# Optimization experiments

Hardware: AMD Instinct MI355X
Metric: run time of the kernel (lower is better)

## Reference

```python
import jax, jax.numpy as jnp
import numpy as np
from jax import lax


def quick_gelu(x):
    return x * jax.nn.sigmoid(1.702 * x)


def setup_inputs() -> dict:
    key = jax.random.key(0)
    ks = jax.random.split(key, 12)
    B, H, W, C, D, M = 32, 56, 56, 192, 64, 8
    g = lambda k, shape, s: (jax.random.normal(k, shape, jnp.float32) * s)
    return {
        "x": jax.random.normal(ks[0], (B, H, W, C), jnp.float32),
        "W1": g(ks[1], (64, C), 0.05),
        "b1": jnp.zeros((64,), jnp.float32),
        "W2": g(ks[2], (64, 64), 0.05),
        "b2": jnp.zeros((64,), jnp.float32),
        "mask_token": g(ks[3], (M, 64), 0.05),
        "Wh": g(ks[4], (D * D * 9, 64), 0.02),
        "bh": g(ks[5], (D * D * 9,), 0.02),
        "Wd": g(ks[6], (D, C), 0.05),
        "bd": jnp.zeros((D,), jnp.float32),
        "Wu": g(ks[7], (C, D), 0.02),
        "bu": jnp.zeros((C,), jnp.float32),
    }


def reference(x, W1, b1, W2, b2, mask_token, Wh, bh, Wd, bd, Wu, bu):
    B, H, W_, C = x.shape
    D = Wd.shape[0]
    M = mask_token.shape[0]
    # meta_net: Linear -> ReLU -> Linear, [B,H,W,64]
    pf = jax.nn.relu(jnp.einsum("bhwc,kc->bhwk", x, W1) + b1)
    pf = jnp.einsum("bhwk,jk->bhwj", pf, W2) + b2
    # mask routing: [M,B,H,W], softmax over spatial positions
    mask = jnp.einsum("bhwk,mk->mbhw", pf, mask_token)
    mask = jax.nn.softmax(mask.reshape(M, B, -1), axis=-1).reshape(M, B, H, W_)
    # sum_m mask[m][...,None]*pf, then sum over H,W -> [B,64]
    mwf = (mask.sum(0)[..., None] * pf).sum(axis=(1, 2))
    # hypernet: per-sample conv weights [B,D,D,3,3]
    conv_w = (jnp.einsum("bk,ok->bo", mwf, Wh) + bh).reshape(B, D, D, 3, 3)
    # adapter_down + QuickGELU, [B,D,H,W]
    xd = jnp.einsum("bhwc,dc->bhwd", x, Wd) + bd
    xp = quick_gelu(xd.transpose(0, 3, 1, 2))

    def conv1(xi, wi):  # xi [D,H,W], wi [D,D,3,3]
        return lax.conv_general_dilated(xi[None], wi, (1, 1), [(1, 1), (1, 1)])[0]

    xc = jax.vmap(conv1)(xp, conv_w)  # [B,D,H,W]
    xd2 = quick_gelu(xc.transpose(0, 2, 3, 1))  # [B,H,W,D]
    # dropout(p=0.1) is identity in eval mode
    xu = jnp.einsum("bhwd,cd->bhwc", xd2, Wu) + bu
    return xu + x
```

## Files before the change

kernel.cpp:

```cpp
#include <hip/hip_runtime.h>

typedef unsigned short ushort_t;
typedef short bf16x8 __attribute__((ext_vector_type(8)));
typedef float f32x4 __attribute__((ext_vector_type(4)));

#define MFMA(a, b, c) __builtin_amdgcn_mfma_f32_16x16x32_bf16(a, b, c, 0, 0, 0)

#define B_    32
#define HW_   3136
#define NPOS  100352

__device__ __forceinline__ float bf2f(unsigned short h) {
    return __uint_as_float(((unsigned int)h) << 16);
}
__device__ __forceinline__ unsigned short f2bf(float f) {
    unsigned int u = __float_as_uint(f);
    u += 0x7FFFu + ((u >> 16) & 1u);
    return (unsigned short)(u >> 16);
}
__device__ __forceinline__ float qgelu(float v) {
    return v / (1.0f + __expf(-1.702f * v));
}
__device__ __forceinline__ void unpack8(uint4 v, float* f) {
    f[0] = bf2f((unsigned short)(v.x & 0xffff)); f[1] = bf2f((unsigned short)(v.x >> 16));
    f[2] = bf2f((unsigned short)(v.y & 0xffff)); f[3] = bf2f((unsigned short)(v.y >> 16));
    f[4] = bf2f((unsigned short)(v.z & 0xffff)); f[5] = bf2f((unsigned short)(v.z >> 16));
    f[6] = bf2f((unsigned short)(v.w & 0xffff)); f[7] = bf2f((unsigned short)(v.w >> 16));
}

__global__ __launch_bounds__(256) void k0_prep(
    const float* __restrict__ W1, const float* __restrict__ W2,
    const float* __restrict__ mtok, const float* __restrict__ Wd,
    const float* __restrict__ Wu,
    ushort_t* __restrict__ w1f, ushort_t* __restrict__ wdf,
    ushort_t* __restrict__ w2f, ushort_t* __restrict__ mtf,
    ushort_t* __restrict__ wuf)
{
    const int gid = blockIdx.x * 256 + threadIdx.x;
    const int stride = gridDim.x * 256;
    for (int i = gid; i < 12288; i += stride) {
        int j = i & 7, lane = (i >> 3) & 63, nt = (i >> 9) & 3, kc = i >> 11;
        int n = nt * 16 + (lane & 15), k = kc * 32 + (lane >> 4) * 8 + j;
        w1f[i] = f2bf(W1[n * 192 + k]);
        wdf[i] = f2bf(Wd[n * 192 + k]);
    }
    for (int i = gid; i < 4096; i += stride) {
        int j = i & 7, lane = (i >> 3) & 63, nt = (i >> 9) & 3, kc = i >> 11;
        int n = nt * 16 + (lane & 15), k = kc * 32 + (lane >> 4) * 8 + j;
        w2f[i] = f2bf(W2[n * 64 + k]);
    }
    for (int i = gid; i < 1024; i += stride) {
        int j = i & 7, lane = (i >> 3) & 63, kc = i >> 9;
        int n = lane & 15, k = kc * 32 + (lane >> 4) * 8 + j;
        mtf[i] = (n < 8) ? f2bf(mtok[n * 64 + k]) : (ushort_t)0;
    }
    for (int i = gid; i < 12288; i += stride) {
        int j = i & 7, lane = (i >> 3) & 63, g = i >> 9;
        int nt = g % 12, kc = g / 12;
        int n = nt * 16 + (lane & 15), k = kc * 32 + (lane >> 4) * 8 + j;
        wuf[i] = f2bf(Wu[n * 64 + k]);
    }
}

__global__ __launch_bounds__(256, 2) void k1_meta_adapter(
    const float* __restrict__ x, const float* __restrict__ b1,
    const float* __restrict__ b2, const float* __restrict__ bd,
    const ushort_t* __restrict__ w1f, const ushort_t* __restrict__ wdf,
    const ushort_t* __restrict__ w2f, const ushort_t* __restrict__ mtf,
    ushort_t* __restrict__ pf2g, ushort_t* __restrict__ xpg,
    float* __restrict__ Lg)
{
    __shared__ ushort_t wsh[29696];
    __shared__ ushort_t buf[4][16 * 72];

    const int tid = threadIdx.x;
    const int lane = tid & 63, wv = tid >> 6;
    const int col = lane & 15, q = lane >> 4;
    const int posBase = blockIdx.x * 64;
    const float* xrow = x + (size_t)(posBase + wv * 16 + col) * 192;

    float4 xv[6][2];
    #pragma unroll
    for (int kc = 0; kc < 6; kc++) {
        const float4* gp = (const float4*)(xrow + kc * 32 + q * 8);
        xv[kc][0] = gp[0]; xv[kc][1] = gp[1];
    }

    {
        uint4* d = (uint4*)wsh;
        const uint4* s1 = (const uint4*)w1f;
        for (int u = tid; u < 1536; u += 256) d[u] = s1[u];
        uint4* d2 = (uint4*)(wsh + 12288);
        const uint4* s2 = (const uint4*)wdf;
        for (int u = tid; u < 1536; u += 256) d2[u] = s2[u];
        uint4* d3 = (uint4*)(wsh + 24576);
        const uint4* s3 = (const uint4*)w2f;
        for (int u = tid; u < 512; u += 256) d3[u] = s3[u];
        uint4* d4 = (uint4*)(wsh + 28672);
        const uint4* s4 = (const uint4*)mtf;
        if (tid < 128) d4[tid] = s4[tid];
    }

    bf16x8 A[6];
    #pragma unroll
    for (int kc = 0; kc < 6; kc++) {
        float4 v0 = xv[kc][0], v1 = xv[kc][1];
        A[kc][0] = (short)f2bf(v0.x); A[kc][1] = (short)f2bf(v0.y);
        A[kc][2] = (short)f2bf(v0.z); A[kc][3] = (short)f2bf(v0.w);
        A[kc][4] = (short)f2bf(v1.x); A[kc][5] = (short)f2bf(v1.y);
        A[kc][6] = (short)f2bf(v1.z); A[kc][7] = (short)f2bf(v1.w);
    }
    __syncthreads();

    f32x4 acc1[4], acc3[4];
    #pragma unroll
    for (int nt = 0; nt < 4; nt++) { acc1[nt] = (f32x4)0.0f; acc3[nt] = (f32x4)0.0f; }

    #pragma unroll
    for (int kc = 0; kc < 6; kc++) {
        #pragma unroll
        for (int nt = 0; nt < 4; nt++) {
            bf16x8 B1 = *(const bf16x8*)&wsh[((kc * 4 + nt) * 64 + lane) * 8];
            acc1[nt] = MFMA(A[kc], B1, acc1[nt]);
            bf16x8 Bd = *(const bf16x8*)&wsh[12288 + ((kc * 4 + nt) * 64 + lane) * 8];
            acc3[nt] = MFMA(A[kc], Bd, acc3[nt]);
        }
    }

    ushort_t* bA = &buf[wv][0];

    #pragma unroll
    for (int nt = 0; nt < 4; nt++) {
        float bias = b1[nt * 16 + col];
        #pragma unroll
        for (int r = 0; r < 4; r++) {
            float v = acc1[nt][r] + bias;
            v = v > 0.0f ? v : 0.0f;
            bA[(q * 4 + r) * 72 + nt * 16 + col] = f2bf(v);
        }
    }

    f32x4 acc2[4];
    #pragma unroll
    for (int nt = 0; nt < 4; nt++) acc2[nt] = (f32x4)0.0f;
    #pragma unroll
    for (int kc = 0; kc < 2; kc++) {
        bf16x8 A2 = *(const bf16x8*)&bA[col * 72 + kc * 32 + q * 8];
        #pragma unroll
        for (int nt = 0; nt < 4; nt++) {
            bf16x8 B2 = *(const bf16x8*)&wsh[24576 + ((kc * 4 + nt) * 64 + lane) * 8];
            acc2[nt] = MFMA(A2, B2, acc2[nt]);
        }
    }

    #pragma unroll
    for (int nt = 0; nt < 4; nt++) {
        float bias = bd[nt * 16 + col];
        #pragma unroll
        for (int r = 0; r < 4; r++) {
            float v = qgelu(acc3[nt][r] + bias);
            bA[(q * 4 + r) * 72 + nt * 16 + col] = f2bf(v);
        }
    }

    #pragma unroll
    for (int t = 0; t < 2; t++) {
        int idx = lane + t * 64;
        int pos = idx >> 3, c8 = idx & 7;
        uint4 vx = *(const uint4*)&bA[pos * 72 + c8 * 8];
        *(uint4*)(xpg + ((size_t)(posBase + wv * 16 + pos)) * 64 + c8 * 8) = vx;
    }

    #pragma unroll
    for (int nt = 0; nt < 4; nt++) {
        float bias = b2[nt * 16 + col];
        #pragma unroll
        for (int r = 0; r < 4; r++)
            bA[(q * 4 + r) * 72 + nt * 16 + col] = f2bf(acc2[nt][r] + bias);
    }

    f32x4 Lacc = (f32x4)0.0f;
    #pragma unroll
    for (int kc = 0; kc < 2; kc++) {
        bf16x8 A3 = *(const bf16x8*)&bA[col * 72 + kc * 32 + q * 8];
        bf16x8 Bm = *(const bf16x8*)&wsh[28672 + (kc * 64 + lane) * 8];
        Lacc = MFMA(A3, Bm, Lacc);
    }
    if (col < 8) {
        #pragma unroll
        for (int r = 0; r < 4; r++)
            Lg[((size_t)(posBase + wv * 16 + q * 4 + r)) * 8 + col] = Lacc[r];
    }

    #pragma unroll
    for (int t = 0; t < 2; t++) {
        int idx = lane + t * 64;
        int pos = idx >> 3, c8 = idx & 7;
        uint4 vp = *(const uint4*)&bA[pos * 72 + c8 * 8];
        *(uint4*)(pf2g + ((size_t)(posBase + wv * 16 + pos)) * 64 + c8 * 8) = vp;
    }
}

__global__ __launch_bounds__(256) void k2a_partial(
    const float* __restrict__ Lg, float* __restrict__ Pmax, float* __restrict__ Psum)
{
    __shared__ float wred[4][8];
    __shared__ float Msh[8];

    const int tid = threadIdx.x;
    const int b = blockIdx.x >> 3, sl = blockIdx.x & 7;
    const int lane = tid & 63, wv = tid >> 6;
    const float* Lb = Lg + ((size_t)b * HW_ + (size_t)sl * 392) * 8;

    float l0[8], l1[8];
    {
        const float4* p = (const float4*)(Lb + (size_t)tid * 8);
        float4 a = p[0], c = p[1];
        l0[0] = a.x; l0[1] = a.y; l0[2] = a.z; l0[3] = a.w;
        l0[4] = c.x; l0[5] = c.y; l0[6] = c.z; l0[7] = c.w;
    }
    if (tid < 136) {
        const float4* p = (const float4*)(Lb + (size_t)(tid + 256) * 8);
        float4 a = p[0], c = p[1];
        l1[0] = a.x; l1[1] = a.y; l1[2] = a.z; l1[3] = a.w;
        l1[4] = c.x; l1[5] = c.y; l1[6] = c.z; l1[7] = c.w;
    } else {
        #pragma unroll
        for (int m = 0; m < 8; m++) l1[m] = -1e30f;
    }

    float lm[8];
    #pragma unroll
    for (int m = 0; m < 8; m++) {
        float v = fmaxf(l0[m], l1[m]);
        for (int off = 32; off > 0; off >>= 1) v = fmaxf(v, __shfl_down(v, off));
        lm[m] = v;
    }
    if (lane == 0) {
        #pragma unroll
        for (int m = 0; m < 8; m++) wred[wv][m] = lm[m];
    }
    __syncthreads();
    if (tid < 8)
        Msh[tid] = fmaxf(fmaxf(wred[0][tid], wred[1][tid]), fmaxf(wred[2][tid], wred[3][tid]));
    __syncthreads();

    float s[8];
    #pragma unroll
    for (int m = 0; m < 8; m++)
        s[m] = __expf(l0[m] - Msh[m]) + __expf(l1[m] - Msh[m]);
    #pragma unroll
    for (int m = 0; m < 8; m++) {
        float v = s[m];
        for (int off = 32; off > 0; off >>= 1) v += __shfl_down(v, off);
        s[m] = v;
    }
    __syncthreads();
    if (lane == 0) {
        #pragma unroll
        for (int m = 0; m < 8; m++) wred[wv][m] = s[m];
    }
    __syncthreads();
    if (tid < 8) {
        Psum[((size_t)b * 8 + sl) * 8 + tid] =
            wred[0][tid] + wred[1][tid] + wred[2][tid] + wred[3][tid];
        Pmax[((size_t)b * 8 + sl) * 8 + tid] = Msh[tid];
    }
}

__global__ __launch_bounds__(256) void k2b_combine(
    const float* __restrict__ Pmax, const float* __restrict__ Psum,
    float* __restrict__ smxg, float* __restrict__ sinvg, float* __restrict__ mwfg)
{
    const int tid = threadIdx.x;
    const int b = tid >> 3, m = tid & 7;
    float M = -1e30f;
    #pragma unroll
    for (int sl = 0; sl < 8; sl++)
        M = fmaxf(M, Pmax[((size_t)b * 8 + sl) * 8 + m]);
    float S = 0.0f;
    #pragma unroll
    for (int sl = 0; sl < 8; sl++)
        S += Psum[((size_t)b * 8 + sl) * 8 + m] * __expf(Pmax[((size_t)b * 8 + sl) * 8 + m] - M);
    smxg[tid] = M;
    sinvg[tid] = 1.0f / S;
    for (int i = tid; i < 2048; i += 256) mwfg[i] = 0.0f;
}

__global__ __launch_bounds__(256) void k2c_mwf(
    const float* __restrict__ Lg, const ushort_t* __restrict__ pf2g,
    const float* __restrict__ smxg, const float* __restrict__ sinvg,
    float* __restrict__ mwfg)
{
    __shared__ float ms[392];
    __shared__ float sred[32 * 64];

    const int tid = threadIdx.x;
    const int b = blockIdx.x >> 3, sl = blockIdx.x & 7;
    const size_t base = (size_t)b * HW_ + (size_t)sl * 392;

    float smx[8], sinv[8];
    #pragma unroll
    for (int m = 0; m < 8; m++) {
        smx[m] = smxg[b * 8 + m];
        sinv[m] = sinvg[b * 8 + m];
    }

    for (int lp = tid; lp < 392; lp += 256) {
        const float4* p = (const float4*)(Lg + (base + lp) * 8);
        float4 a = p[0], c = p[1];
        ms[lp] = __expf(a.x - smx[0]) * sinv[0] + __expf(a.y - smx[1]) * sinv[1]
               + __expf(a.z - smx[2]) * sinv[2] + __expf(a.w - smx[3]) * sinv[3]
               + __expf(c.x - smx[4]) * sinv[4] + __expf(c.y - smx[5]) * sinv[5]
               + __expf(c.z - smx[6]) * sinv[6] + __expf(c.w - smx[7]) * sinv[7];
    }
    __syncthreads();

    const int part = tid >> 3, kg = tid & 7;
    float a8[8];
    #pragma unroll
    for (int j = 0; j < 8; j++) a8[j] = 0.0f;
    for (int lp = part; lp < 392; lp += 32) {
        float w = ms[lp];
        uint4 v = *(const uint4*)(pf2g + (base + lp) * 64 + kg * 8);
        float f[8]; unpack8(v, f);
        #pragma unroll
        for (int j = 0; j < 8; j++) a8[j] += w * f[j];
    }
    #pragma unroll
    for (int j = 0; j < 8; j++) sred[part * 64 + kg * 8 + j] = a8[j];
    __syncthreads();
    if (tid < 64) {
        float s = 0.0f;
        #pragma unroll
        for (int pt = 0; pt < 32; pt++) s += sred[pt * 64 + tid];
        atomicAdd(&mwfg[b * 64 + tid], s);
    }
}

__global__ __launch_bounds__(256) void k3_hypernet(
    const float* __restrict__ mwfg, const float* __restrict__ Whg,
    const float* __restrict__ bhg, ushort_t* __restrict__ cwb)
{
    __shared__ float mwfs[32 * 64];
    const int tid = threadIdx.x;
    for (int i = tid; i < 2048; i += 256) mwfs[i] = mwfg[i];
    __syncthreads();

    const int op = blockIdx.x * 64 + (tid >> 2);
    const int bq = tid & 3;
    const int j = op & 7, lane = (op >> 3) & 63, nt = (op >> 9) & 3;
    const int kc = (op >> 11) & 1, tap = op >> 12;
    const int oc = nt * 16 + (lane & 15);
    const int ic = kc * 32 + (lane >> 4) * 8 + j;
    const int o = oc * 576 + ic * 9 + tap;

    float wreg[64];
    const float4* src = (const float4*)(Whg + (size_t)o * 64);
    #pragma unroll
    for (int t = 0; t < 16; t++) {
        float4 v = src[t];
        wreg[t * 4 + 0] = v.x; wreg[t * 4 + 1] = v.y;
        wreg[t * 4 + 2] = v.z; wreg[t * 4 + 3] = v.w;
    }
    const float bias = bhg[o];
    #pragma unroll
    for (int i = 0; i < 8; i += 2) {
        int b0 = bq * 8 + i, b1 = b0 + 1;
        float a0 = bias, a1 = bias;
        #pragma unroll
        for (int k = 0; k < 64; k++) {
            a0 += mwfs[b0 * 64 + k] * wreg[k];
            a1 += mwfs[b1 * 64 + k] * wreg[k];
        }
        cwb[(size_t)b0 * 36864 + op] = f2bf(a0);
        cwb[(size_t)b1 * 36864 + op] = f2bf(a1);
    }
}

__global__ __launch_bounds__(256, 4) void k4_conv(
    const ushort_t* __restrict__ xpg, const ushort_t* __restrict__ cwb,
    ushort_t* __restrict__ xd2g)
{
    __shared__ ushort_t xs[2 * 232 * 40];

    const int tid = threadIdx.x;
    const int bid = blockIdx.x;
    const int swz = (bid & 7) * 112 + (bid >> 3);
    const int b = swz / 28, yt = swz % 28, y0 = yt * 2;

    for (int u = tid; u < 1856; u += 256) {
        int r = u / 464, rem = u % 464, c = rem >> 3, c8 = rem & 7;
        int gy = y0 - 1 + r, gx = c - 1;
        uint4 v = make_uint4(0, 0, 0, 0);
        if (gy >= 0 && gy < 56 && gx >= 0 && gx < 56)
            v = *(const uint4*)(xpg + ((size_t)b * HW_ + gy * 56 + gx) * 64 + c8 * 8);
        int kc = c8 >> 2, q = c8 & 3;
        *(uint4*)&xs[kc * 9280 + (r * 58 + c) * 40 + q * 8] = v;
    }
    __syncthreads();

    const int lane = tid & 63, wv = tid >> 6;
    const int col = lane & 15, q = lane >> 4;

    int abase[7];
    #pragma unroll
    for (int t = 0; t < 7; t++) {
        int p = t * 16 + col;
        int row = p / 56, cc = p - row * 56;
        abase[t] = ((row * 58 + cc) * 40 + q * 8) * 2;
    }

    f32x4 acc[7];
    #pragma unroll
    for (int t = 0; t < 7; t++) acc[t] = (f32x4)0.0f;

    const ushort_t* wbase = cwb + (size_t)b * 36864;
    #pragma unroll
    for (int tap = 0; tap < 9; tap++) {
        const int dy = tap / 3, dx = tap % 3;
        const int toff = (dy * 58 + dx) * 80;
        bf16x8 Bf0 = *(const bf16x8*)(wbase + tap * 4096 + ((0 * 4 + wv) * 64 + lane) * 8);
        bf16x8 Bf1 = *(const bf16x8*)(wbase + tap * 4096 + ((1 * 4 + wv) * 64 + lane) * 8);
        #pragma unroll
        for (int t = 0; t < 7; t++) {
            bf16x8 A0 = *(const bf16x8*)((const char*)xs + abase[t] + toff);
            bf16x8 A1 = *(const bf16x8*)((const char*)xs + 18560 + abase[t] + toff);
            acc[t] = MFMA(A0, Bf0, acc[t]);
            acc[t] = MFMA(A1, Bf1, acc[t]);
        }
    }
    __syncthreads();

    #pragma unroll
    for (int t = 0; t < 7; t++)
        #pragma unroll
        for (int r = 0; r < 4; r++)
            xs[(t * 16 + q * 4 + r) * 72 + wv * 16 + col] = f2bf(qgelu(acc[t][r]));
    __syncthreads();

    for (int u = tid; u < 896; u += 256) {
        int pos = u >> 3, c8 = u & 7;
        uint4 v = *(const uint4*)&xs[pos * 72 + c8 * 8];
        size_t gpos = (size_t)b * HW_ + (size_t)y0 * 56 + pos;
        *(uint4*)(xd2g + gpos * 64 + c8 * 8) = v;
    }
}

__global__ __launch_bounds__(256, 4) void k5_up_res(
    const ushort_t* __restrict__ xd2g, const ushort_t* __restrict__ wuf,
    const float* __restrict__ bu, const float* __restrict__ xg,
    float* __restrict__ outg)
{
    __shared__ ushort_t xds[64 * 72];
    __shared__ ushort_t wsh[12288];

    const int tid = threadIdx.x;
    const size_t posBase = (size_t)blockIdx.x * 64;

    {
        uint4* d = (uint4*)wsh;
        const uint4* s = (const uint4*)wuf;
        for (int u = tid; u < 1536; u += 256) d[u] = s[u];
    }
    #pragma unroll
    for (int t = 0; t < 2; t++) {
        int u = tid + t * 256;
        int pos = u >> 3, c8 = u & 7;
        uint4 v = *(const uint4*)(xd2g + (posBase + pos) * 64 + c8 * 8);
        *(uint4*)&xds[pos * 72 + c8 * 8] = v;
    }
    __syncthreads();

    const int lane = tid & 63, wv = tid >> 6;
    const int col = lane & 15, q = lane >> 4;

    bf16x8 A[2];
    #pragma unroll
    for (int kc = 0; kc < 2; kc++)
        A[kc] = *(const bf16x8*)&xds[(wv * 16 + col) * 72 + kc * 32 + q * 8];

    f32x4 acc[12];
    #pragma unroll
    for (int nt = 0; nt < 12; nt++) acc[nt] = (f32x4)0.0f;
    #pragma unroll
    for (int kc = 0; kc < 2; kc++)
        #pragma unroll
        for (int nt = 0; nt < 12; nt++) {
            bf16x8 B = *(const bf16x8*)&wsh[((kc * 12 + nt) * 64 + lane) * 8];
            acc[nt] = MFMA(A[kc], B, acc[nt]);
        }

    #pragma unroll
    for (int nt = 0; nt < 12; nt++) {
        float bias = bu[nt * 16 + col];
        #pragma unroll
        for (int r = 0; r < 4; r++) {
            size_t off = (posBase + wv * 16 + q * 4 + r) * 192 + nt * 16 + col;
            outg[off] = acc[nt][r] + bias + xg[off];
        }
    }
}

extern "C" void kernel_launch(void* const* d_in, const int* in_sizes, int n_in,
                              void* d_out, int out_size, void* d_ws, size_t ws_size,
                              hipStream_t stream) {
    const float* x    = (const float*)d_in[0];
    const float* W1   = (const float*)d_in[1];
    const float* b1   = (const float*)d_in[2];
    const float* W2   = (const float*)d_in[3];
    const float* b2   = (const float*)d_in[4];
    const float* mtok = (const float*)d_in[5];
    const float* Wh   = (const float*)d_in[6];
    const float* bh   = (const float*)d_in[7];
    const float* Wd   = (const float*)d_in[8];
    const float* bd   = (const float*)d_in[9];
    const float* Wu   = (const float*)d_in[10];
    const float* bu   = (const float*)d_in[11];
    float* out = (float*)d_out;

    char* ws = (char*)d_ws;
    ushort_t* pf2 = (ushort_t*)ws;
    ushort_t* xp  = (ushort_t*)(ws + 12845056);
    ushort_t* xd2 = pf2;
    ushort_t* cwb = (ushort_t*)(ws + 25690112);
    float*    mwf = (float*)(ws + 28049408);
    float*    Lg  = (float*)(ws + 28057600);
    ushort_t* w1f = (ushort_t*)(ws + 31268864);
    ushort_t* wdf = (ushort_t*)(ws + 31293440);
    ushort_t* w2f = (ushort_t*)(ws + 31318016);
    ushort_t* mtf = (ushort_t*)(ws + 31326208);
    ushort_t* wuf = (ushort_t*)(ws + 31328256);
    float*    Pmax= (float*)(ws + 31352832);
    float*    Psum= (float*)(ws + 31361024);
    float*    smxg= (float*)(ws + 31369216);
    float*    sinvg=(float*)(ws + 31370240);

    k0_prep<<<48, 256, 0, stream>>>(W1, W2, mtok, Wd, Wu, w1f, wdf, w2f, mtf, wuf);
    k1_meta_adapter<<<1568, 256, 0, stream>>>(x, b1, b2, bd, w1f, wdf, w2f, mtf,
                                              pf2, xp, Lg);
    k2a_partial<<<256, 256, 0, stream>>>(Lg, Pmax, Psum);
    k2b_combine<<<1, 256, 0, stream>>>(Pmax, Psum, smxg, sinvg, mwf);
    k2c_mwf<<<256, 256, 0, stream>>>(Lg, pf2, smxg, sinvg, mwf);
    k3_hypernet<<<576, 256, 0, stream>>>(mwf, Wh, bh, cwb);
    k4_conv<<<896, 256, 0, stream>>>(xp, cwb, xd2);
    k5_up_res<<<1568, 256, 0, stream>>>(xd2, wuf, bu, x, out);
}
```

Before: 248.0 us.

## Process 64 positions per single-wave block, reading weights directly from global

Kernel k1 now launches one 64-thread wave per block. That wave handles all four 16-row M tiles and reuses each loaded weight fragment across four MFMAs, instead of staging about 59KB of weights in shared memory per 256-thread block. This removes the per-block LDS weight copy and the __syncthreads, and lowers LDS use so more blocks can be resident. In exchange, each wave holds 32 f32x4 accumulators, which raises register pressure. Weight reads now rely on L1/L2 caching, and each block has only one wave, so there are fewer waves to hide latency.

```diff
diff --git a/kernel.cpp b/kernel.cpp
--- a/kernel.cpp
+++ b/kernel.cpp
@@ -62,7 +62,7 @@
     }
 }
 
-__global__ __launch_bounds__(256, 2) void k1_meta_adapter(
+__global__ __launch_bounds__(64, 2) void k1_meta_adapter(
     const float* __restrict__ x, const float* __restrict__ b1,
     const float* __restrict__ b2, const float* __restrict__ bd,
     const ushort_t* __restrict__ w1f, const ushort_t* __restrict__ wdf,
@@ -70,134 +70,118 @@
     ushort_t* __restrict__ pf2g, ushort_t* __restrict__ xpg,
     float* __restrict__ Lg)
 {
-    __shared__ ushort_t wsh[29696];
-    __shared__ ushort_t buf[4][16 * 72];
-
-    const int tid = threadIdx.x;
-    const int lane = tid & 63, wv = tid >> 6;
+    __shared__ ushort_t buf[16 * 72];
+
+    const int lane = threadIdx.x;
     const int col = lane & 15, q = lane >> 4;
     const int posBase = blockIdx.x * 64;
-    const float* xrow = x + (size_t)(posBase + wv * 16 + col) * 192;
-
-    float4 xv[6][2];
+
+    float bias1[4], biasd[4], bias2[4];
+    #pragma unroll
+    for (int nt = 0; nt < 4; nt++) {
+        bias1[nt] = b1[nt * 16 + col];
+        biasd[nt] = bd[nt * 16 + col];
+        bias2[nt] = b2[nt * 16 + col];
+    }
+
+    f32x4 acc1[4][4], acc3[4][4];
+    #pragma unroll
+    for (int m = 0; m < 4; m++)
+        #pragma unroll
+        for (int nt = 0; nt < 4; nt++) { acc1[m][nt] = (f32x4)0.0f; acc3[m][nt] = (f32x4)0.0f; }
+
     #pragma unroll
     for (int kc = 0; kc < 6; kc++) {
-        const float4* gp = (const float4*)(xrow + kc * 32 + q * 8);
-        xv[kc][0] = gp[0]; xv[kc][1] = gp[1];
-    }
-
-    {
-        uint4* d = (uint4*)wsh;
-        const uint4* s1 = (const uint4*)w1f;
-        for (int u = tid; u < 1536; u += 256) d[u] = s1[u];
-        uint4* d2 = (uint4*)(wsh + 12288);
-        const uint4* s2 = (const uint4*)wdf;
-        for (int u = tid; u < 1536; u += 256) d2[u] = s2[u];
-        uint4* d3 = (uint4*)(wsh + 24576);
-        const uint4* s3 = (const uint4*)w2f;
-        for (int u = tid; u < 512; u += 256) d3[u] = s3[u];
-        uint4* d4 = (uint4*)(wsh + 28672);
-        const uint4* s4 = (const uint4*)mtf;
-        if (tid < 128) d4[tid] = s4[tid];
-    }
-
-    bf16x8 A[6];
-    #pragma unroll
-    for (int kc = 0; kc < 6; kc++) {
-        float4 v0 = xv[kc][0], v1 = xv[kc][1];
-        A[kc][0] = (short)f2bf(v0.x); A[kc][1] = (short)f2bf(v0.y);
-        A[kc][2] = (short)f2bf(v0.z); A[kc][3] = (short)f2bf(v0.w);
-        A[kc][4] = (short)f2bf(v1.x); A[kc][5] = (short)f2bf(v1.y);
-        A[kc][6] = (short)f2bf(v1.z); A[kc][7] = (short)f2bf(v1.w);
-    }
-    __syncthreads();
-
-    f32x4 acc1[4], acc3[4];
-    #pragma unroll
-    for (int nt = 0; nt < 4; nt++) { acc1[nt] = (f32x4)0.0f; acc3[nt] = (f32x4)0.0f; }
-
-    #pragma unroll
-    for (int kc = 0; kc < 6; kc++) {
+        bf16x8 A[4];
+        #pragma unroll
+        for (int m = 0; m < 4; m++) {
+            const float4* gp = (const float4*)(x +
+                (size_t)(posBase + m * 16 + col) * 192 + kc * 32 + q * 8);
+            float4 v0 = gp[0], v1 = gp[1];
+            A[m][0] = (short)f2bf(v0.x); A[m][1] = (short)f2bf(v0.y);
+            A[m][2] = (short)f2bf(v0.z); A[m][3] = (short)f2bf(v0.w);
+            A[m][4] = (short)f2bf(v1.x); A[m][5] = (short)f2bf(v1.y);
+            A[m][6] = (short)f2bf(v1.z); A[m][7] = (short)f2bf(v1.w);
+        }
         #pragma unroll
         for (int nt = 0; nt < 4; nt++) {
-            bf16x8 B1 = *(const bf16x8*)&wsh[((kc * 4 + nt) * 64 + lane) * 8];
-            acc1[nt] = MFMA(A[kc], B1, acc1[nt]);
-            bf16x8 Bd = *(const bf16x8*)&wsh[12288 + ((kc * 4 + nt) * 64 + lane) * 8];
-            acc3[nt] = MFMA(A[kc], Bd, acc3[nt]);
-        }
-    }
-
-    ushort_t* bA = &buf[wv][0];
-
-    #pragma unroll
-    for (int nt = 0; nt < 4; nt++) {
-        float bias = b1[nt * 16 + col];
-        #pragma unroll
-        for (int r = 0; r < 4; r++) {
-            float v = acc1[nt][r] + bias;
-            v = v > 0.0f ? v : 0.0f;
-            bA[(q * 4 + r) * 72 + nt * 16 + col] = f2bf(v);
-        }
-    }
-
-    f32x4 acc2[4];
-    #pragma unroll
-    for (int nt = 0; nt < 4; nt++) acc2[nt] = (f32x4)0.0f;
-    #pragma unroll
-    for (int kc = 0; kc < 2; kc++) {
-        bf16x8 A2 = *(const bf16x8*)&bA[col * 72 + kc * 32 + q * 8];
-        #pragma unroll
-        for (int nt = 0; nt < 4; nt++) {
-            bf16x8 B2 = *(const bf16x8*)&wsh[24576 + ((kc * 4 + nt) * 64 + lane) * 8];
-            acc2[nt] = MFMA(A2, B2, acc2[nt]);
-        }
-    }
-
-    #pragma unroll
-    for (int nt = 0; nt < 4; nt++) {
-        float bias = bd[nt * 16 + col];
-        #pragma unroll
-        for (int r = 0; r < 4; r++) {
-            float v = qgelu(acc3[nt][r] + bias);
-            bA[(q * 4 + r) * 72 + nt * 16 + col] = f2bf(v);
-        }
-    }
-
-    #pragma unroll
-    for (int t = 0; t < 2; t++) {
-        int idx = lane + t * 64;
-        int pos = idx >> 3, c8 = idx & 7;
-        uint4 vx = *(const uint4*)&bA[pos * 72 + c8 * 8];
-        *(uint4*)(xpg + ((size_t)(posBase + wv * 16 + pos)) * 64 + c8 * 8) = vx;
-    }
-
-    #pragma unroll
-    for (int nt = 0; nt < 4; nt++) {
-        float bias = b2[nt * 16 + col];
-        #pragma unroll
-        for (int r = 0; r < 4; r++)
-            bA[(q * 4 + r) * 72 + nt * 16 + col] = f2bf(acc2[nt][r] + bias);
-    }
-
-    f32x4 Lacc = (f32x4)0.0f;
-    #pragma unroll
-    for (int kc = 0; kc < 2; kc++) {
-        bf16x8 A3 = *(const bf16x8*)&bA[col * 72 + kc * 32 + q * 8];
-        bf16x8 Bm = *(const bf16x8*)&wsh[28672 + (kc * 64 + lane) * 8];
-        Lacc = MFMA(A3, Bm, Lacc);
-    }
-    if (col < 8) {
-        #pragma unroll
-        for (int r = 0; r < 4; r++)
-            Lg[((size_t)(posBase + wv * 16 + q * 4 + r)) * 8 + col] = Lacc[r];
-    }
-
-    #pragma unroll
-    for (int t = 0; t < 2; t++) {
-        int idx = lane + t * 64;
-        int pos = idx >> 3, c8 = idx & 7;
-        uint4 vp = *(const uint4*)&bA[pos * 72 + c8 * 8];
-        *(uint4*)(pf2g + ((size_t)(posBase + wv * 16 + pos)) * 64 + c8 * 8) = vp;
+            bf16x8 B1 = *(const bf16x8*)(w1f + ((kc * 4 + nt) * 64 + lane) * 8);
+            #pragma unroll
+            for (int m = 0; m < 4; m++) acc1[m][nt] = MFMA(A[m], B1, acc1[m][nt]);
+            bf16x8 Bd = *(const bf16x8*)(wdf + ((kc * 4 + nt) * 64 + lane) * 8);
+            #pragma unroll
+            for (int m = 0; m < 4; m++) acc3[m][nt] = MFMA(A[m], Bd, acc3[m][nt]);
+        }
+    }
+
+    #pragma unroll
+    for (int m = 0; m < 4; m++) {
+        const int rowBase = posBase + m * 16;
+
+        #pragma unroll
+        for (int nt = 0; nt < 4; nt++)
+            #pragma unroll
+            for (int r = 0; r < 4; r++) {
+                float v = acc1[m][nt][r] + bias1[nt];
+                v = v > 0.0f ? v : 0.0f;
+                buf[(q * 4 + r) * 72 + nt * 16 + col] = f2bf(v);
+            }
+
+        f32x4 acc2[4];
+        #pragma unroll
+        for (int nt = 0; nt < 4; nt++) acc2[nt] = (f32x4)0.0f;
+        #pragma unroll
+        for (int kc = 0; kc < 2; kc++) {
+            bf16x8 A2 = *(const bf16x8*)&buf[col * 72 + kc * 32 + q * 8];
+            #pragma unroll
+            for (int nt = 0; nt < 4; nt++) {
+                bf16x8 B2 = *(const bf16x8*)(w2f + ((kc * 4 + nt) * 64 + lane) * 8);
+                acc2[nt] = MFMA(A2, B2, acc2[nt]);
+            }
+        }
+
+        #pragma unroll
+        for (int nt = 0; nt < 4; nt++)
+            #pragma unroll
+            for (int r = 0; r < 4; r++) {
+                float v = qgelu(acc3[m][nt][r] + biasd[nt]);
+                buf[(q * 4 + r) * 72 + nt * 16 + col] = f2bf(v);
+            }
+
+        #pragma unroll
+        for (int t = 0; t < 2; t++) {
+            int idx = lane + t * 64;
+            int pos = idx >> 3, c8 = idx & 7;
+            uint4 vx = *(const uint4*)&buf[pos * 72 + c8 * 8];
+            *(uint4*)(xpg + ((size_t)(rowBase + pos)) * 64 + c8 * 8) = vx;
+        }
+
+        #pragma unroll
+        for (int nt = 0; nt < 4; nt++)
+            #pragma unroll
+            for (int r = 0; r < 4; r++)
+                buf[(q * 4 + r) * 72 + nt * 16 + col] = f2bf(acc2[nt][r] + bias2[nt]);
+
+        f32x4 Lacc = (f32x4)0.0f;
+        #pragma unroll
+        for (int kc = 0; kc < 2; kc++) {
+            bf16x8 A3 = *(const bf16x8*)&buf[col * 72 + kc * 32 + q * 8];
+            bf16x8 Bm = *(const bf16x8*)(mtf + (kc * 64 + lane) * 8);
+            Lacc = MFMA(A3, Bm, Lacc);
+        }
+        if (col < 8) {
+            #pragma unroll
+            for (int r = 0; r < 4; r++)
+                Lg[((size_t)(rowBase + q * 4 + r)) * 8 + col] = Lacc[r];
+        }
+
+        #pragma unroll
+        for (int t = 0; t < 2; t++) {
+            int idx = lane + t * 64;
+            int pos = idx >> 3, c8 = idx & 7;
+            uint4 vp = *(const uint4*)&buf[pos * 72 + c8 * 8];
+            *(uint4*)(pf2g + ((size_t)(rowBase + pos)) * 64 + c8 * 8) = vp;
+        }
     }
 }
 
@@ -537,8 +521,8 @@
     float*    sinvg=(float*)(ws + 31370240);
 
     k0_prep<<<48, 256, 0, stream>>>(W1, W2, mtok, Wd, Wu, w1f, wdf, w2f, mtf, wuf);
-    k1_meta_adapter<<<1568, 256, 0, stream>>>(x, b1, b2, bd, w1f, wdf, w2f, mtf,
-                                              pf2, xp, Lg);
+    k1_meta_adapter<<<1568, 64, 0, stream>>>(x, b1, b2, bd, w1f, wdf, w2f, mtf,
+                                             pf2, xp, Lg);
     k2a_partial<<<256, 256, 0, stream>>>(Lg, Pmax, Psum);
     k2b_combine<<<1, 256, 0, stream>>>(Pmax, Psum, smxg, sinvg, mwf);
     k2c_mwf<<<256, 256, 0, stream>>>(Lg, pf2, smxg, sinvg, mwf);
```

New measurement: 241.3 us. -2.7%, faster.
